# Performance work log

Measured on AMD Instinct MI355X. Metric: run time of the kernel, lower is better.

The kernel has to match this reference:

```python
import jax, jax.numpy as jnp
import numpy as np

H = 32       # num attention heads
KV = 8       # num key/value heads
D = 128      # head dim
HID = 4096   # hidden size
EPS = 1e-6
THETA = 1000000.0


def _rms_norm(x, w, eps=EPS):
    xf = x.astype(jnp.float32)
    var = jnp.mean(xf * xf, axis=-1, keepdims=True)
    return (w * (xf * jax.lax.rsqrt(var + eps)).astype(x.dtype))


def _rotate_half(x):
    x1, x2 = jnp.split(x, 2, axis=-1)
    return jnp.concatenate((-x2, x1), axis=-1)


def setup_inputs() -> dict:
    key = jax.random.key(0)
    ks = jax.random.split(key, 8)
    B, S = 1, 2048
    hidden_states = jax.random.normal(ks[0], (B, S, HID), dtype=jnp.float32)
    # causal additive mask [B,1,S,S]
    neg = jnp.finfo(jnp.float32).min
    causal = jnp.where(jnp.tril(jnp.ones((S, S), dtype=bool)), 0.0, neg)
    attention_mask = causal[None, None, :, :].astype(jnp.float32)
    position_ids = jnp.arange(S, dtype=jnp.int64 if jax.config.jax_enable_x64 else jnp.int32)[None, :]
    scale = 0.02
    Wq = jax.random.normal(ks[1], (H * D, HID), dtype=jnp.float32) * scale
    Wk = jax.random.normal(ks[2], (KV * D, HID), dtype=jnp.float32) * scale
    Wv = jax.random.normal(ks[3], (KV * D, HID), dtype=jnp.float32) * scale
    Wo = jax.random.normal(ks[4], (HID, H * D), dtype=jnp.float32) * scale
    q_norm_w = jnp.ones((D,), dtype=jnp.float32)
    k_norm_w = jnp.ones((D,), dtype=jnp.float32)
    return {"hidden_states": hidden_states, "attention_mask": attention_mask,
            "position_ids": position_ids, "Wq": Wq, "Wk": Wk, "Wv": Wv,
            "Wo": Wo, "q_norm_w": q_norm_w, "k_norm_w": k_norm_w}


def reference(hidden_states, attention_mask, position_ids, Wq, Wk, Wv, Wo, q_norm_w, k_norm_w):
    B, S, _ = hidden_states.shape
    dtype = hidden_states.dtype
    # QKV projections (Linear, no bias): y = x @ W.T
    q = (hidden_states @ Wq.T).reshape(B, S, H, D).transpose(0, 2, 1, 3)    # [B,H,S,D]
    k = (hidden_states @ Wk.T).reshape(B, S, KV, D).transpose(0, 2, 1, 3)   # [B,KV,S,D]
    v = (hidden_states @ Wv.T).reshape(B, S, KV, D).transpose(0, 2, 1, 3)   # [B,KV,S,D]
    # per-head RMSNorm on head_dim
    q = _rms_norm(q, q_norm_w)
    k = _rms_norm(k, k_norm_w)
    # rotary embeddings
    inv_freq = 1.0 / (THETA ** (jnp.arange(0, D, 2, dtype=jnp.float32) / D))   # [D/2]
    freqs = position_ids.astype(jnp.float32)[:, :, None] * inv_freq[None, None, :]  # [B,S,D/2]
    emb = jnp.concatenate((freqs, freqs), axis=-1)                               # [B,S,D]
    cos = jnp.cos(emb).astype(dtype)[:, None, :, :]   # [B,1,S,D]
    sin = jnp.sin(emb).astype(dtype)[:, None, :, :]
    q = q * cos + _rotate_half(q) * sin
    k = k * cos + _rotate_half(k) * sin
    # GQA: repeat kv heads
    n_rep = H // KV
    k = jnp.repeat(k, n_rep, axis=1)   # [B,H,S,D]
    v = jnp.repeat(v, n_rep, axis=1)
    # attention
    scores = jnp.einsum('bhqd,bhkd->bhqk', q, k) / np.sqrt(D).astype(np.float32)
    scores = scores + attention_mask
    probs = jax.nn.softmax(scores.astype(jnp.float32), axis=-1).astype(dtype)
    ctx = jnp.einsum('bhqk,bhkd->bhqd', probs, v)           # [B,H,S,D]
    ctx = ctx.transpose(0, 2, 1, 3).reshape(B, S, H * D)    # [B,S,H*D]
    return ctx @ Wo.T
```

## Files before the change

kernel.cpp:

```cpp
#include <hip/hip_runtime.h>
#include <hip/hip_bf16.h>
#include <math.h>

typedef unsigned short u16;
typedef __attribute__((ext_vector_type(8))) __bf16 bf16x8;
typedef __attribute__((ext_vector_type(4))) float f32x4;

#define DEV static __device__ __forceinline__

DEV float bf2f(u16 b) { union { unsigned u; float f; } c; c.u = ((unsigned)b) << 16; return c.f; }
DEV u16 f2bf(float f) {
    union { float f; unsigned u; } c; c.f = f;
    return (u16)((c.u + 0x7fffu + ((c.u >> 16) & 1u)) >> 16);
}

DEV void gl_lds16(const void* g, void* l) {
    __builtin_amdgcn_global_load_lds((__attribute__((address_space(1))) void*)(void*)g,
                                     (__attribute__((address_space(3))) void*)l, 16, 0, 0);
}

__global__ __launch_bounds__(256) void k_cvt(const float* __restrict__ in, u16* __restrict__ out, int n) {
    int stride = gridDim.x * blockDim.x;
    for (int i = blockIdx.x * blockDim.x + threadIdx.x; i * 4 < n; i += stride) {
        float4 v = *(const float4*)(in + (size_t)i * 4);
        ushort4 o = make_ushort4(f2bf(v.x), f2bf(v.y), f2bf(v.z), f2bf(v.w));
        *(ushort4*)(out + (size_t)i * 4) = o;
    }
}

template<int OUT_BF16>
__global__ __launch_bounds__(256) void k_gemm(const u16* __restrict__ A, const u16* __restrict__ B,
                                              void* __restrict__ Cv, int N, int K) {
    __shared__ u16 sA[128 * 64];
    __shared__ u16 sB[128 * 64];
    const int tid = threadIdx.x;
    const int lane = tid & 63, wid = tid >> 6;
    const int wr = wid >> 1, wc = wid & 1;
    const int l15 = lane & 15, l4 = lane >> 4;
    const long mBase = (long)blockIdx.y * 128;
    const long nBase = (long)blockIdx.x * 128;

    f32x4 acc[4][4] = {};

    const int r0 = tid >> 3;
    const int s0 = tid & 7;

    for (int k0 = 0; k0 < K; k0 += 64) {
#pragma unroll
        for (int i = 0; i < 4; ++i) {
            int row = i * 32 + r0;
            int srcs = s0 ^ (row & 7);
            gl_lds16(A + (mBase + row) * (long)K + k0 + srcs * 8, (char*)sA + (i * 256 + tid) * 16);
            gl_lds16(B + (nBase + row) * (long)K + k0 + srcs * 8, (char*)sB + (i * 256 + tid) * 16);
        }
        __syncthreads();
#pragma unroll
        for (int kk = 0; kk < 2; ++kk) {
            bf16x8 av[4], bv[4];
#pragma unroll
            for (int mi = 0; mi < 4; ++mi) {
                int row = wr * 64 + mi * 16 + l15;
                int off = (kk * 64 + l4 * 16) ^ ((row & 7) << 4);
                av[mi] = *(const bf16x8*)((const char*)sA + row * 128 + off);
            }
#pragma unroll
            for (int ni = 0; ni < 4; ++ni) {
                int row = wc * 64 + ni * 16 + l15;
                int off = (kk * 64 + l4 * 16) ^ ((row & 7) << 4);
                bv[ni] = *(const bf16x8*)((const char*)sB + row * 128 + off);
            }
#pragma unroll
            for (int mi = 0; mi < 4; ++mi)
#pragma unroll
                for (int ni = 0; ni < 4; ++ni)
                    acc[mi][ni] = __builtin_amdgcn_mfma_f32_16x16x32_bf16(av[mi], bv[ni], acc[mi][ni], 0, 0, 0);
        }
        __syncthreads();
    }

#pragma unroll
    for (int mi = 0; mi < 4; ++mi) {
#pragma unroll
        for (int ni = 0; ni < 4; ++ni) {
#pragma unroll
            for (int r = 0; r < 4; ++r) {
                long row = mBase + wr * 64 + mi * 16 + l4 * 4 + r;
                long col = nBase + wc * 64 + ni * 16 + l15;
                float v = acc[mi][ni][r];
                if (OUT_BF16) ((u16*)Cv)[row * N + col] = f2bf(v);
                else          ((float*)Cv)[row * N + col] = v;
            }
        }
    }
}

__global__ __launch_bounds__(256) void k_nrope(const u16* __restrict__ QKV, const int* __restrict__ pos,
                                               const float* __restrict__ qw, const float* __restrict__ kw,
                                               u16* __restrict__ Qr, u16* __restrict__ Kr, u16* __restrict__ Vt) {
    const int s = blockIdx.x;
    const int tid = threadIdx.x;
    const int g = tid >> 5, l32 = tid & 31;
    const int d0 = l32 * 4;
    const float p = (float)pos[s];
    float cs[4], sn[4];
#pragma unroll
    for (int i = 0; i < 4; ++i) {
        int j = (d0 + i) & 63;
        float inv = exp2f(-0.31143075889569023f * (float)j);
        float fr = p * inv;
        cs[i] = cosf(fr);
        sn[i] = sinf(fr);
    }
    const bool low = (d0 < 64);

    for (int r = g; r < 40; r += 8) {
        const bool isQ = r < 32;
        const int h = isQ ? r : r - 32;
        const u16* src = QKV + (long)s * 6144 + (isQ ? h * 128 : 4096 + h * 128) + d0;
        ushort4 xv = *(const ushort4*)src;
        float x0 = bf2f(xv.x), x1 = bf2f(xv.y), x2 = bf2f(xv.z), x3 = bf2f(xv.w);
        float ss = x0 * x0 + x1 * x1 + x2 * x2 + x3 * x3;
#pragma unroll
        for (int off = 16; off >= 1; off >>= 1) ss += __shfl_xor(ss, off, 64);
        float rms = rsqrtf(ss * (1.0f / 128.0f) + 1e-6f);
        const float* w = isQ ? qw : kw;
        float n0 = x0 * rms * w[d0 + 0];
        float n1 = x1 * rms * w[d0 + 1];
        float n2 = x2 * rms * w[d0 + 2];
        float n3 = x3 * rms * w[d0 + 3];
        float o0 = __shfl_xor(n0, 16, 64);
        float o1 = __shfl_xor(n1, 16, 64);
        float o2 = __shfl_xor(n2, 16, 64);
        float o3 = __shfl_xor(n3, 16, 64);
        float y0 = low ? n0 * cs[0] - o0 * sn[0] : n0 * cs[0] + o0 * sn[0];
        float y1 = low ? n1 * cs[1] - o1 * sn[1] : n1 * cs[1] + o1 * sn[1];
        float y2 = low ? n2 * cs[2] - o2 * sn[2] : n2 * cs[2] + o2 * sn[2];
        float y3 = low ? n3 * cs[3] - o3 * sn[3] : n3 * cs[3] + o3 * sn[3];
        ushort4 ov = make_ushort4(f2bf(y0), f2bf(y1), f2bf(y2), f2bf(y3));
        u16* dst = (isQ ? Qr + ((long)h * 2048 + s) * 128 : Kr + ((long)h * 2048 + s) * 128) + d0;
        *(ushort4*)dst = ov;
    }
    {
        const u16* src = QKV + (long)s * 6144 + 5120 + g * 128 + d0;
        ushort4 v = *(const ushort4*)src;
        u16* base = Vt + ((long)g * 128 + d0) * 2048 + s;
        base[0] = v.x; base[2048] = v.y; base[4096] = v.z; base[6144] = v.w;
    }
}

__global__ __launch_bounds__(256) void k_attn(const u16* __restrict__ Qr, const u16* __restrict__ Kr,
                                              const u16* __restrict__ Vt, u16* __restrict__ ctx) {
    __shared__ char sK[32 * 256];
    __shared__ char sV[128 * 64];
    __shared__ char sP[4 * 16 * 64];
    const int qb = blockIdx.x, h = blockIdx.y;
    const int kvh = h >> 2;
    const int tid = threadIdx.x, wid = tid >> 6, lane = tid & 63;
    const int l15 = lane & 15, l4 = lane >> 4;
    const int qrow = qb * 64 + wid * 16 + l15;
    const u16* qsrc = Qr + ((long)h * 2048 + qrow) * 128;
    bf16x8 aq[4];
#pragma unroll
    for (int kk = 0; kk < 4; ++kk) aq[kk] = *(const bf16x8*)(qsrc + kk * 32 + l4 * 8);

    f32x4 o[8] = {};
    float m[4] = {-3e38f, -3e38f, -3e38f, -3e38f};
    float lsum[4] = {0.f, 0.f, 0.f, 0.f};
    const int kvmax = qb * 64 + 63;
    const int wqbase = qb * 64 + wid * 16;
    const long Kh = (long)kvh * 2048 * 128;
    const long Vh = (long)kvh * 128 * 2048;

    for (int kv0 = 0; kv0 <= kvmax; kv0 += 32) {
#pragma unroll
        for (int i = 0; i < 2; ++i) {
            int lin = i * 256 + tid;
            int row = lin >> 4, slot = lin & 15;
            gl_lds16(Kr + Kh + ((long)(kv0 + row)) * 128 + (slot ^ (row & 7)) * 8, sK + lin * 16);
            int d = lin >> 2, sl2 = lin & 3;
            gl_lds16(Vt + Vh + (long)d * 2048 + kv0 + (sl2 ^ (d & 3)) * 8, sV + lin * 16);
        }
        __syncthreads();
        if (kv0 <= wqbase + 15) {
            f32x4 sj[2];
#pragma unroll
            for (int j = 0; j < 2; ++j) {
                f32x4 sacc = {};
#pragma unroll
                for (int kk = 0; kk < 4; ++kk) {
                    int row = j * 16 + l15;
                    int off = (kk * 64 + l4 * 16) ^ ((row & 7) << 4);
                    bf16x8 bk = *(const bf16x8*)(sK + row * 256 + off);
                    sacc = __builtin_amdgcn_mfma_f32_16x16x32_bf16(aq[kk], bk, sacc, 0, 0, 0);
                }
                int kg = kv0 + j * 16 + l15;
#pragma unroll
                for (int r = 0; r < 4; ++r) {
                    int qg = wqbase + l4 * 4 + r;
                    sacc[r] = (kg <= qg) ? sacc[r] * 0.08838834764831845f : -3e38f;
                }
                sj[j] = sacc;
            }
            float fac[4];
#pragma unroll
            for (int r = 0; r < 4; ++r) {
                float pm = fmaxf(sj[0][r], sj[1][r]);
                pm = fmaxf(pm, __shfl_xor(pm, 1, 64));
                pm = fmaxf(pm, __shfl_xor(pm, 2, 64));
                pm = fmaxf(pm, __shfl_xor(pm, 4, 64));
                pm = fmaxf(pm, __shfl_xor(pm, 8, 64));
                float mn = fmaxf(m[r], pm);
                fac[r] = __expf(m[r] - mn);
                m[r] = mn;
            }
#pragma unroll
            for (int di = 0; di < 8; ++di)
#pragma unroll
                for (int r = 0; r < 4; ++r) o[di][r] *= fac[r];
#pragma unroll
            for (int r = 0; r < 4; ++r) {
                int q = l4 * 4 + r;
                float e0 = __expf(sj[0][r] - m[r]);
                float e1 = __expf(sj[1][r] - m[r]);
                int base = wid * 1024 + q * 64;
                *(u16*)(sP + base + ((2 * l15) ^ ((q & 3) << 4))) = f2bf(e0);
                *(u16*)(sP + base + ((32 + 2 * l15) ^ ((q & 3) << 4))) = f2bf(e1);
                float ps = e0 + e1;
                ps += __shfl_xor(ps, 1, 64);
                ps += __shfl_xor(ps, 2, 64);
                ps += __shfl_xor(ps, 4, 64);
                ps += __shfl_xor(ps, 8, 64);
                lsum[r] = lsum[r] * fac[r] + ps;
            }
            asm volatile("s_waitcnt lgkmcnt(0)" ::: "memory");
            bf16x8 pa = *(const bf16x8*)(sP + wid * 1024 + l15 * 64 + ((l4 * 16) ^ ((l15 & 3) << 4)));
#pragma unroll
            for (int di = 0; di < 8; ++di) {
                int vr = di * 16 + l15;
                int off = (l4 * 16) ^ ((vr & 3) << 4);
                bf16x8 bv = *(const bf16x8*)(sV + vr * 64 + off);
                o[di] = __builtin_amdgcn_mfma_f32_16x16x32_bf16(pa, bv, o[di], 0, 0, 0);
            }
        }
        __syncthreads();
    }
    float inv[4];
#pragma unroll
    for (int r = 0; r < 4; ++r) inv[r] = 1.0f / lsum[r];
#pragma unroll
    for (int di = 0; di < 8; ++di) {
#pragma unroll
        for (int r = 0; r < 4; ++r) {
            long row = wqbase + l4 * 4 + r;
            ctx[row * 4096 + h * 128 + di * 16 + l15] = f2bf(o[di][r] * inv[r]);
        }
    }
}

extern "C" void kernel_launch(void* const* d_in, const int* in_sizes, int n_in,
                              void* d_out, int out_size, void* d_ws, size_t ws_size,
                              hipStream_t stream) {
    const float* hs = (const float*)d_in[0];
    const int* pos = (const int*)d_in[2];
    const float* Wq = (const float*)d_in[3];
    const float* Wk = (const float*)d_in[4];
    const float* Wv = (const float*)d_in[5];
    const float* Wo = (const float*)d_in[6];
    const float* qw = (const float*)d_in[7];
    const float* kw = (const float*)d_in[8];

    u16* base = (u16*)d_ws;
    u16* X16   = base;
    u16* W16   = X16 + 8388608;
    u16* Wo16  = W16 + 25165824;
    u16* QKV16 = Wo16 + 16777216;
    u16* Qh    = QKV16 + 12582912;
    u16* Kh    = Qh + 8388608;
    u16* Vh    = Kh + 2097152;
    u16* ctx   = Vh + 2097152;

    dim3 blk(256);
    k_cvt<<<2048, blk, 0, stream>>>(hs, X16, 8388608);
    k_cvt<<<2048, blk, 0, stream>>>(Wq, W16, 16777216);
    k_cvt<<<2048, blk, 0, stream>>>(Wk, W16 + 16777216, 4194304);
    k_cvt<<<2048, blk, 0, stream>>>(Wv, W16 + 20971520, 4194304);
    k_cvt<<<2048, blk, 0, stream>>>(Wo, Wo16, 16777216);

    k_gemm<1><<<dim3(48, 16), blk, 0, stream>>>(X16, W16, (void*)QKV16, 6144, 4096);
    k_nrope<<<2048, blk, 0, stream>>>(QKV16, pos, qw, kw, Qh, Kh, Vh);
    k_attn<<<dim3(32, 32), blk, 0, stream>>>(Qh, Kh, Vh, ctx);
    k_gemm<0><<<dim3(32, 16), blk, 0, stream>>>(ctx, Wo16, d_out, 4096, 4096);
}
```

Measured before the change: 672.6 us.

## Restructure attention with paired causal q-tiles, double-buffered 64-wide KV, lazy rescale

Each attention block now handles two query tiles (i and 31-i) so causal work is balanced across blocks and K/V tiles are shared between them. KV tiles grow to 64 rows and are double-buffered, with the next tile's async global-to-LDS load issued before computing the current one. The softmax scale is folded into Q during the norm/rope pass, and causal masking is applied only on diagonal tiles. Rescaling of the running max is skipped unless the new max exceeds the old one by more than 8, which lets the exponentials run against a stale max. The costs are higher LDS use and register pressure from two accumulator sets, and only half as many blocks are launched.

```diff
diff --git a/kernel.cpp b/kernel.cpp
--- a/kernel.cpp
+++ b/kernel.cpp
@@ -136,6 +136,10 @@
         float y1 = low ? n1 * cs[1] - o1 * sn[1] : n1 * cs[1] + o1 * sn[1];
         float y2 = low ? n2 * cs[2] - o2 * sn[2] : n2 * cs[2] + o2 * sn[2];
         float y3 = low ? n3 * cs[3] - o3 * sn[3] : n3 * cs[3] + o3 * sn[3];
+        if (isQ) {
+            const float sc = 0.08838834764831845f;
+            y0 *= sc; y1 *= sc; y2 *= sc; y3 *= sc;
+        }
         ushort4 ov = make_ushort4(f2bf(y0), f2bf(y1), f2bf(y2), f2bf(y3));
         u16* dst = (isQ ? Qr + ((long)h * 2048 + s) * 128 : Kr + ((long)h * 2048 + s) * 128) + d0;
         *(ushort4*)dst = ov;
@@ -150,109 +154,144 @@
 
 __global__ __launch_bounds__(256) void k_attn(const u16* __restrict__ Qr, const u16* __restrict__ Kr,
                                               const u16* __restrict__ Vt, u16* __restrict__ ctx) {
-    __shared__ char sK[32 * 256];
-    __shared__ char sV[128 * 64];
-    __shared__ char sP[4 * 16 * 64];
-    const int qb = blockIdx.x, h = blockIdx.y;
+    __shared__ char sK[2][64 * 256];
+    __shared__ char sV[2][128 * 128];
+    __shared__ char sP[4][2048];
+    const int pairIdx = blockIdx.x, h = blockIdx.y;
     const int kvh = h >> 2;
+    const int qb[2] = {pairIdx, 31 - pairIdx};
     const int tid = threadIdx.x, wid = tid >> 6, lane = tid & 63;
     const int l15 = lane & 15, l4 = lane >> 4;
-    const int qrow = qb * 64 + wid * 16 + l15;
-    const u16* qsrc = Qr + ((long)h * 2048 + qrow) * 128;
-    bf16x8 aq[4];
-#pragma unroll
-    for (int kk = 0; kk < 4; ++kk) aq[kk] = *(const bf16x8*)(qsrc + kk * 32 + l4 * 8);
-
-    f32x4 o[8] = {};
-    float m[4] = {-3e38f, -3e38f, -3e38f, -3e38f};
-    float lsum[4] = {0.f, 0.f, 0.f, 0.f};
-    const int kvmax = qb * 64 + 63;
-    const int wqbase = qb * 64 + wid * 16;
+
+    bf16x8 aq[2][4];
+    f32x4 o[2][8] = {};
+    float m[2][4], lsum[2][4];
+#pragma unroll
+    for (int tI = 0; tI < 2; ++tI) {
+        int qrow = qb[tI] * 64 + wid * 16 + l15;
+        const u16* qsrc = Qr + ((long)h * 2048 + qrow) * 128;
+#pragma unroll
+        for (int kk = 0; kk < 4; ++kk) aq[tI][kk] = *(const bf16x8*)(qsrc + kk * 32 + l4 * 8);
+#pragma unroll
+        for (int r = 0; r < 4; ++r) { m[tI][r] = -3e38f; lsum[tI][r] = 0.f; }
+    }
     const long Kh = (long)kvh * 2048 * 128;
     const long Vh = (long)kvh * 128 * 2048;
-
-    for (int kv0 = 0; kv0 <= kvmax; kv0 += 32) {
-#pragma unroll
-        for (int i = 0; i < 2; ++i) {
+    const int nt = qb[1] + 1;
+
+    auto STAGE = [&](int buf, int t) {
+        int kv0 = t * 64;
+#pragma unroll
+        for (int i = 0; i < 4; ++i) {
             int lin = i * 256 + tid;
-            int row = lin >> 4, slot = lin & 15;
-            gl_lds16(Kr + Kh + ((long)(kv0 + row)) * 128 + (slot ^ (row & 7)) * 8, sK + lin * 16);
-            int d = lin >> 2, sl2 = lin & 3;
-            gl_lds16(Vt + Vh + (long)d * 2048 + kv0 + (sl2 ^ (d & 3)) * 8, sV + lin * 16);
-        }
-        __syncthreads();
-        if (kv0 <= wqbase + 15) {
-            f32x4 sj[2];
-#pragma unroll
-            for (int j = 0; j < 2; ++j) {
+            int krow = lin >> 4, kslot = lin & 15;
+            gl_lds16(Kr + Kh + (long)(kv0 + krow) * 128 + (kslot ^ (krow & 7)) * 8, sK[buf] + lin * 16);
+            int d = lin >> 3, vslot = lin & 7;
+            gl_lds16(Vt + Vh + (long)d * 2048 + kv0 + (vslot ^ (d & 7)) * 8, sV[buf] + lin * 16);
+        }
+    };
+
+    STAGE(0, 0);
+    __syncthreads();
+    int cur = 0;
+    for (int t = 0; t < nt; ++t) {
+        if (t + 1 < nt) STAGE(cur ^ 1, t + 1);
+#pragma unroll
+        for (int tI = 0; tI < 2; ++tI) {
+            if (t > qb[tI]) continue;
+            const int wq = qb[tI] * 64 + wid * 16;
+            const bool diag = (t == qb[tI]);
+            f32x4 sj[4];
+#pragma unroll
+            for (int j = 0; j < 4; ++j) {
                 f32x4 sacc = {};
 #pragma unroll
                 for (int kk = 0; kk < 4; ++kk) {
                     int row = j * 16 + l15;
                     int off = (kk * 64 + l4 * 16) ^ ((row & 7) << 4);
-                    bf16x8 bk = *(const bf16x8*)(sK + row * 256 + off);
-                    sacc = __builtin_amdgcn_mfma_f32_16x16x32_bf16(aq[kk], bk, sacc, 0, 0, 0);
+                    bf16x8 bk = *(const bf16x8*)(sK[cur] + row * 256 + off);
+                    sacc = __builtin_amdgcn_mfma_f32_16x16x32_bf16(aq[tI][kk], bk, sacc, 0, 0, 0);
                 }
-                int kg = kv0 + j * 16 + l15;
-#pragma unroll
-                for (int r = 0; r < 4; ++r) {
-                    int qg = wqbase + l4 * 4 + r;
-                    sacc[r] = (kg <= qg) ? sacc[r] * 0.08838834764831845f : -3e38f;
+                if (diag) {
+                    int kg = t * 64 + j * 16 + l15;
+#pragma unroll
+                    for (int r = 0; r < 4; ++r)
+                        sacc[r] = (kg <= wq + l4 * 4 + r) ? sacc[r] : -3e38f;
                 }
                 sj[j] = sacc;
             }
-            float fac[4];
+            float pm[4];
+            bool need = false;
 #pragma unroll
             for (int r = 0; r < 4; ++r) {
-                float pm = fmaxf(sj[0][r], sj[1][r]);
-                pm = fmaxf(pm, __shfl_xor(pm, 1, 64));
-                pm = fmaxf(pm, __shfl_xor(pm, 2, 64));
-                pm = fmaxf(pm, __shfl_xor(pm, 4, 64));
-                pm = fmaxf(pm, __shfl_xor(pm, 8, 64));
-                float mn = fmaxf(m[r], pm);
-                fac[r] = __expf(m[r] - mn);
-                m[r] = mn;
-            }
-#pragma unroll
-            for (int di = 0; di < 8; ++di)
-#pragma unroll
-                for (int r = 0; r < 4; ++r) o[di][r] *= fac[r];
+                float v = fmaxf(fmaxf(sj[0][r], sj[1][r]), fmaxf(sj[2][r], sj[3][r]));
+                v = fmaxf(v, __shfl_xor(v, 1, 64));
+                v = fmaxf(v, __shfl_xor(v, 2, 64));
+                v = fmaxf(v, __shfl_xor(v, 4, 64));
+                v = fmaxf(v, __shfl_xor(v, 8, 64));
+                pm[r] = v;
+                need = need || (v > m[tI][r] + 8.f);
+            }
+            if (__any(need)) {
+#pragma unroll
+                for (int r = 0; r < 4; ++r) {
+                    float mn = fmaxf(m[tI][r], pm[r]);
+                    float fac = __expf(m[tI][r] - mn);
+                    m[tI][r] = mn;
+                    lsum[tI][r] *= fac;
+#pragma unroll
+                    for (int di = 0; di < 8; ++di) o[tI][di][r] *= fac;
+                }
+            }
+            char* sPw = sP[wid];
 #pragma unroll
             for (int r = 0; r < 4; ++r) {
                 int q = l4 * 4 + r;
-                float e0 = __expf(sj[0][r] - m[r]);
-                float e1 = __expf(sj[1][r] - m[r]);
-                int base = wid * 1024 + q * 64;
-                *(u16*)(sP + base + ((2 * l15) ^ ((q & 3) << 4))) = f2bf(e0);
-                *(u16*)(sP + base + ((32 + 2 * l15) ^ ((q & 3) << 4))) = f2bf(e1);
-                float ps = e0 + e1;
+                int swz = ((q & 7) ^ ((q >> 3) << 1)) << 4;
+                float ps = 0.f;
+#pragma unroll
+                for (int j = 0; j < 4; ++j) {
+                    float e = __expf(sj[j][r] - m[tI][r]);
+                    ps += e;
+                    *(u16*)(sPw + q * 128 + ((j * 32 + l15 * 2) ^ swz)) = f2bf(e);
+                }
                 ps += __shfl_xor(ps, 1, 64);
                 ps += __shfl_xor(ps, 2, 64);
                 ps += __shfl_xor(ps, 4, 64);
                 ps += __shfl_xor(ps, 8, 64);
-                lsum[r] = lsum[r] * fac[r] + ps;
+                lsum[tI][r] += ps;
             }
             asm volatile("s_waitcnt lgkmcnt(0)" ::: "memory");
-            bf16x8 pa = *(const bf16x8*)(sP + wid * 1024 + l15 * 64 + ((l4 * 16) ^ ((l15 & 3) << 4)));
+            int pswz = ((l15 & 7) ^ ((l15 >> 3) << 1)) << 4;
+            bf16x8 pa0 = *(const bf16x8*)(sPw + l15 * 128 + ((l4 * 16) ^ pswz));
+            bf16x8 pa1 = *(const bf16x8*)(sPw + l15 * 128 + ((64 + l4 * 16) ^ pswz));
 #pragma unroll
             for (int di = 0; di < 8; ++di) {
                 int vr = di * 16 + l15;
-                int off = (l4 * 16) ^ ((vr & 3) << 4);
-                bf16x8 bv = *(const bf16x8*)(sV + vr * 64 + off);
-                o[di] = __builtin_amdgcn_mfma_f32_16x16x32_bf16(pa, bv, o[di], 0, 0, 0);
+                int voff = (l4 * 16) ^ ((vr & 7) << 4);
+                bf16x8 bv0 = *(const bf16x8*)(sV[cur] + vr * 128 + voff);
+                bf16x8 bv1 = *(const bf16x8*)(sV[cur] + vr * 128 + (voff ^ 64));
+                o[tI][di] = __builtin_amdgcn_mfma_f32_16x16x32_bf16(pa0, bv0, o[tI][di], 0, 0, 0);
+                o[tI][di] = __builtin_amdgcn_mfma_f32_16x16x32_bf16(pa1, bv1, o[tI][di], 0, 0, 0);
             }
         }
         __syncthreads();
-    }
-    float inv[4];
-#pragma unroll
-    for (int r = 0; r < 4; ++r) inv[r] = 1.0f / lsum[r];
-#pragma unroll
-    for (int di = 0; di < 8; ++di) {
-#pragma unroll
-        for (int r = 0; r < 4; ++r) {
-            long row = wqbase + l4 * 4 + r;
-            ctx[row * 4096 + h * 128 + di * 16 + l15] = f2bf(o[di][r] * inv[r]);
+        cur ^= 1;
+    }
+
+#pragma unroll
+    for (int tI = 0; tI < 2; ++tI) {
+        float inv[4];
+#pragma unroll
+        for (int r = 0; r < 4; ++r) inv[r] = 1.0f / lsum[tI][r];
+        int wq = qb[tI] * 64 + wid * 16;
+#pragma unroll
+        for (int di = 0; di < 8; ++di) {
+#pragma unroll
+            for (int r = 0; r < 4; ++r) {
+                long row = wq + l4 * 4 + r;
+                ctx[row * 4096 + h * 128 + di * 16 + l15] = f2bf(o[tI][di][r] * inv[r]);
+            }
         }
     }
 }
@@ -288,6 +327,6 @@
 
     k_gemm<1><<<dim3(48, 16), blk, 0, stream>>>(X16, W16, (void*)QKV16, 6144, 4096);
     k_nrope<<<2048, blk, 0, stream>>>(QKV16, pos, qw, kw, Qh, Kh, Vh);
-    k_attn<<<dim3(32, 32), blk, 0, stream>>>(Qh, Kh, Vh, ctx);
+    k_attn<<<dim3(16, 32), blk, 0, stream>>>(Qh, Kh, Vh, ctx);
     k_gemm<0><<<dim3(32, 16), blk, 0, stream>>>(ctx, Wo16, d_out, 4096, 4096);
 }
```

Result: faster. 596.7 us (-11.3%).
